# Optimization experiments

Measured on AMD Instinct MI355X. Metric: run time of the kernel, lower is better.

Reference implementation:

```python
import jax, jax.numpy as jnp
import numpy as np

EMBED_DIM = 1024
NUM_HEADS = 16
HEAD_DIM = EMBED_DIM // NUM_HEADS


def setup_inputs() -> dict:
    key = jax.random.key(0)
    k_x, k_wqkv, k_bqkv, k_wo, k_bo = jax.random.split(key, 5)
    b, n = 2, 2048
    scale_in = 1.0 / np.sqrt(EMBED_DIM)
    return {
        "x": jax.random.normal(k_x, (b, n, EMBED_DIM), dtype=jnp.float32),
        "W_qkv": jax.random.normal(k_wqkv, (EMBED_DIM, 3 * EMBED_DIM), dtype=jnp.float32) * scale_in,
        "b_qkv": jnp.zeros((3 * EMBED_DIM,), dtype=jnp.float32),
        "W_out": jax.random.normal(k_wo, (EMBED_DIM, EMBED_DIM), dtype=jnp.float32) * scale_in,
        "b_out": jnp.zeros((EMBED_DIM,), dtype=jnp.float32),
    }


def _rope_rotate(t, cos, sin):
    # t: [b, h, n, hd]; cos/sin: [1, 1, n, hd//2]
    t1, t2 = jnp.split(t, 2, axis=-1)
    return jnp.concatenate([cos * t1 - sin * t2, sin * t1 + cos * t2], axis=-1)


def reference(x, W_qkv, b_qkv, W_out, b_out):
    b, n, d = x.shape
    h, hd = NUM_HEADS, HEAD_DIM

    qkv = x @ W_qkv + b_qkv                      # [b, n, 3d]
    q, k, v = jnp.split(qkv, 3, axis=-1)
    q, k, v = [t.reshape(b, n, h, hd).transpose(0, 2, 1, 3) for t in (q, k, v)]

    # RoPE tables
    hd2 = hd // 2
    theta = 10000.0 ** (-2.0 * jnp.arange(hd2, dtype=jnp.float32) / hd)
    freqs = jnp.arange(n, dtype=jnp.float32)[:, None] * theta[None, :]  # [n, hd2]
    cos = jnp.cos(freqs)[None, None]
    sin = jnp.sin(freqs)[None, None]
    q = _rope_rotate(q, cos, sin)
    k = _rope_rotate(k, cos, sin)

    scores = jnp.einsum('bhqd,bhkd->bhqk', q, k) / jnp.sqrt(jnp.float32(hd))
    attn = jax.nn.softmax(scores, axis=-1)       # [b, h, n, n]
    out = jnp.einsum('bhqk,bhkd->bhqd', attn, v)
    out = out.transpose(0, 2, 1, 3).reshape(b, n, d)
    return out @ W_out + b_out
```

## Files before the change

kernel.cpp:

```cpp
#include <hip/hip_runtime.h>
#include <hip/hip_bf16.h>
#include <math.h>

#define EMBED 1024
#define NHEAD 16
#define HD 64
#define BATCH 2
#define SEQ 2048
#define MTOT (BATCH * SEQ)
#define QKVN (3 * EMBED)

typedef __attribute__((ext_vector_type(8))) short short8;
typedef __attribute__((ext_vector_type(4))) float f32x4;

typedef __attribute__((address_space(1))) const unsigned int GUI;
typedef __attribute__((address_space(3))) unsigned int LUI;

__device__ __forceinline__ void gload_lds16(const void* src, void* dst) {
  __builtin_amdgcn_global_load_lds((GUI*)src, (LUI*)dst, 16, 0, 0);
}

__device__ __forceinline__ unsigned short f2bf(float f) {
  unsigned u = __builtin_bit_cast(unsigned, f);
  u += 0x7fffu + ((u >> 16) & 1u);
  return (unsigned short)(u >> 16);
}

__device__ __forceinline__ unsigned cvt_pk_bf16(float lo, float hi) {
  unsigned r;
  asm("v_cvt_pk_bf16_f32 %0, %1, %2" : "=v"(r) : "v"(lo), "v"(hi));
  return r;
}

#define QSCALE 0.1803368801111191f


__global__ __launch_bounds__(256) void k_cvt(const float* __restrict__ in,
                                             unsigned short* __restrict__ out, int n4) {
  int i = blockIdx.x * 256 + threadIdx.x;
  if (i >= n4) return;
  float4 v = reinterpret_cast<const float4*>(in)[i];
  ushort4 o;
  o.x = f2bf(v.x); o.y = f2bf(v.y); o.z = f2bf(v.z); o.w = f2bf(v.w);
  reinterpret_cast<ushort4*>(out)[i] = o;
}

__global__ __launch_bounds__(256) void k_transpose_cvt(const float* __restrict__ W,
                                                       unsigned short* __restrict__ WT,
                                                       int K, int Ncols) {
  __shared__ float tile[32][33];
  int n0 = blockIdx.x * 32, k0 = blockIdx.y * 32;
  int tc = threadIdx.x & 31, tr = threadIdx.x >> 5;
  for (int i = 0; i < 4; i++) {
    int r = tr + i * 8;
    tile[r][tc] = W[(size_t)(k0 + r) * Ncols + n0 + tc];
  }
  __syncthreads();
  for (int i = 0; i < 4; i++) {
    int r = tr + i * 8;
    WT[(size_t)(n0 + r) * K + k0 + tc] = f2bf(tile[tc][r]);
  }
}

__global__ __launch_bounds__(256) void k_rope_tables(float* __restrict__ cosT,
                                                     float* __restrict__ sinT) {
  int idx = blockIdx.x * 256 + threadIdx.x;
  if (idx >= SEQ * 32) return;
  int pos = idx >> 5, i = idx & 31;
  float theta = __expf((float)i * -0.28782313662425575f);
  float f = (float)pos * theta;
  cosT[idx] = cosf(f);
  sinT[idx] = sinf(f);
}

__device__ __forceinline__ void gemm_mainloop(const unsigned short* __restrict__ A,
                                              const unsigned short* __restrict__ Bt,
                                              unsigned short* Al, unsigned short* Bl,
                                              size_t m0, size_t n0,
                                              int tid, int l15, int g, int wm, int wn,
                                              f32x4 acc[4][4]) {
  const int w = tid >> 6;
  const int lane = tid & 63;
  const int srow = lane >> 3, slot = lane & 7;
  for (int k0 = 0; k0 < 1024; k0 += 64) {
    __syncthreads();
    for (int it = 0; it < 4; it++) {
      const int r = w * 32 + it * 8 + srow;
      const int sc = (slot ^ (r & 7)) * 8;
      gload_lds16(A + (m0 + r) * 1024 + k0 + sc, &Al[(w * 32 + it * 8) * 64]);
      gload_lds16(Bt + (n0 + r) * 1024 + k0 + sc, &Bl[(w * 32 + it * 8) * 64]);
    }
    __syncthreads();
    for (int kk = 0; kk < 2; kk++) {
      short8 fa[4], fb[4];
      const int xr = ((kk * 4 + g) ^ (l15 & 7)) * 8;
      for (int i = 0; i < 4; i++)
        fa[i] = *reinterpret_cast<const short8*>(&Al[(wm * 64 + i * 16 + l15) * 64 + xr]);
      for (int j = 0; j < 4; j++)
        fb[j] = *reinterpret_cast<const short8*>(&Bl[(wn * 64 + j * 16 + l15) * 64 + xr]);
      for (int i = 0; i < 4; i++)
        for (int j = 0; j < 4; j++)
          acc[i][j] = __builtin_amdgcn_mfma_f32_16x16x32_bf16(fa[i], fb[j], acc[i][j], 0, 0, 0);
    }
  }
}

__global__ __launch_bounds__(256) void k_qkv_gemm(const unsigned short* __restrict__ A,
                                                  const unsigned short* __restrict__ Bt,
                                                  const float* __restrict__ bias,
                                                  const float* __restrict__ cosT,
                                                  const float* __restrict__ sinT,
                                                  unsigned short* __restrict__ Qb,
                                                  unsigned short* __restrict__ Kb,
                                                  unsigned short* __restrict__ Vtg) {
  __shared__ alignas(16) unsigned short Al[128 * 64];
  __shared__ alignas(16) unsigned short Bl[128 * 64];
  const int tid = threadIdx.x;
  const int lane = tid & 63, l15 = lane & 15, g = lane >> 4;
  const int wid = tid >> 6, wm = wid >> 1, wn = wid & 1;
  const size_t m0 = (size_t)blockIdx.y * 128;
  const size_t n0 = (size_t)blockIdx.x * 128;
  f32x4 acc[4][4] = {};
  gemm_mainloop(A, Bt, Al, Bl, m0, n0, tid, l15, g, wm, wn, acc);

  const int cbase = (int)n0 + wn * 64;
  const int sec = cbase >> 10;
  const int head = (cbase & 1023) >> 6;
  float bia[4];
  for (int j = 0; j < 4; j++) bia[j] = bias[cbase + j * 16 + l15];
  const size_t mw = m0 + wm * 64;

  if (sec == 2) {
    const int dsw = ((l15 >> 3) & 1) << 2;
    for (int i = 0; i < 4; i++) {
      size_t mbase = mw + i * 16 + g * 4;
      int bb = (int)(mbase >> 11), pos0 = (int)(mbase & 2047);
      size_t hb = (size_t)(bb * NHEAD + head) * HD;
      for (int j = 0; j < 4; j++) {
        int d = j * 16 + l15;
        uint2 pk;
        pk.x = cvt_pk_bf16(acc[i][j][0] + bia[j], acc[i][j][1] + bia[j]);
        pk.y = cvt_pk_bf16(acc[i][j][2] + bia[j], acc[i][j][3] + bia[j]);
        *reinterpret_cast<uint2*>(Vtg + (hb + d) * SEQ + (pos0 ^ dsw)) = pk;
      }
    }
  } else {
    unsigned short* dst = sec ? Kb : Qb;
    const float qs = sec ? 1.0f : QSCALE;
    for (int i = 0; i < 4; i++)
      for (int r = 0; r < 4; r++) {
        size_t m = mw + i * 16 + g * 4 + r;
        int bb = (int)(m >> 11), pos = (int)(m & 2047);
        size_t base = ((size_t)(bb * NHEAD + head) * SEQ + pos) * HD;
        const float* cr = cosT + pos * 32;
        const float* sr = sinT + pos * 32;
        for (int pl = 0; pl < 2; pl++) {
          int ii = pl * 16 + l15;
          float c = cr[ii], s = sr[ii];
          float lo = acc[i][pl][r] + bia[pl];
          float hi = acc[i][pl + 2][r] + bia[pl + 2];
          dst[base + ii]      = f2bf((c * lo - s * hi) * qs);
          dst[base + 32 + ii] = f2bf((s * lo + c * hi) * qs);
        }
      }
  }
}

__global__ __launch_bounds__(256) void k_out_gemm(const unsigned short* __restrict__ A,
                                                  const unsigned short* __restrict__ Bt,
                                                  const float* __restrict__ bias,
                                                  float* __restrict__ out) {
  __shared__ alignas(16) unsigned short Al[128 * 64];
  __shared__ alignas(16) unsigned short Bl[64 * 64];
  const int tid = threadIdx.x;
  const int lane = tid & 63, l15 = lane & 15, g = lane >> 4;
  const int wid = tid >> 6, wm = wid >> 1, wn = wid & 1;
  const int w = wid;
  const int srow = lane >> 3, slot = lane & 7;
  const size_t m0 = (size_t)blockIdx.y * 128;
  const size_t n0 = (size_t)blockIdx.x * 64;
  f32x4 acc[4][2] = {};

  for (int k0 = 0; k0 < 1024; k0 += 64) {
    __syncthreads();
    for (int it = 0; it < 4; it++) {
      const int r = w * 32 + it * 8 + srow;
      const int sc = (slot ^ (r & 7)) * 8;
      gload_lds16(A + (m0 + r) * 1024 + k0 + sc, &Al[(w * 32 + it * 8) * 64]);
    }
    for (int it = 0; it < 2; it++) {
      const int r = w * 16 + it * 8 + srow;
      const int sc = (slot ^ (r & 7)) * 8;
      gload_lds16(Bt + (n0 + r) * 1024 + k0 + sc, &Bl[(w * 16 + it * 8) * 64]);
    }
    __syncthreads();
    for (int kk = 0; kk < 2; kk++) {
      short8 fa[4], fb[2];
      const int xr = ((kk * 4 + g) ^ (l15 & 7)) * 8;
      for (int i = 0; i < 4; i++)
        fa[i] = *reinterpret_cast<const short8*>(&Al[(wm * 64 + i * 16 + l15) * 64 + xr]);
      for (int j = 0; j < 2; j++)
        fb[j] = *reinterpret_cast<const short8*>(&Bl[(wn * 32 + j * 16 + l15) * 64 + xr]);
      for (int i = 0; i < 4; i++)
        for (int j = 0; j < 2; j++)
          acc[i][j] = __builtin_amdgcn_mfma_f32_16x16x32_bf16(fa[i], fb[j], acc[i][j], 0, 0, 0);
    }
  }

  const int cbase = (int)n0 + wn * 32;
  const size_t mw = m0 + wm * 64;
  for (int i = 0; i < 4; i++)
    for (int r = 0; r < 4; r++) {
      size_t m = mw + i * 16 + g * 4 + r;
      for (int j = 0; j < 2; j++) {
        int col = cbase + j * 16 + l15;
        out[m * EMBED + col] = acc[i][j][r] + bias[col];
      }
    }
}

__global__ __launch_bounds__(256) void k_attn(const unsigned short* __restrict__ Q,
                                              const unsigned short* __restrict__ Kg,
                                              const unsigned short* __restrict__ Vtg,
                                              unsigned short* __restrict__ AO) {
  __shared__ alignas(16) unsigned short Kt[64 * 64];
  __shared__ alignas(16) unsigned short Vt[64 * 64];
  const int tid = threadIdx.x, w = tid >> 6, lane = tid & 63;
  const int l15 = lane & 15, g = lane >> 4;
  const int srow = lane >> 3, slot = lane & 7;
  const int bh = blockIdx.y;
  const unsigned short* Qp = Q + (size_t)bh * SEQ * HD;
  const unsigned short* Kp = Kg + (size_t)bh * SEQ * HD;
  const unsigned short* Vp = Vtg + (size_t)bh * HD * SEQ;
  const int q0 = blockIdx.x * 64 + w * 16;

  short8 aq[2];
  for (int kk = 0; kk < 2; kk++)
    aq[kk] = *reinterpret_cast<const short8*>(Qp + (size_t)(q0 + l15) * HD + kk * 32 + g * 8);

  f32x4 o[4] = {};
  float mrow = -INFINITY, lrow = 0.f;

  for (int t = 0; t < SEQ / 64; t++) {
    const int kb = t * 64;
    __syncthreads();
    for (int it = 0; it < 2; it++) {
      const int r = w * 16 + it * 8 + srow;
      const int sc = (slot ^ (r & 7)) * 8;
      gload_lds16(Kp + (size_t)(kb + r) * HD + sc, &Kt[(w * 16 + it * 8) * 64]);
      gload_lds16(Vp + (size_t)r * SEQ + kb + sc, &Vt[(w * 16 + it * 8) * 64]);
    }
    __syncthreads();

    f32x4 s[4] = {};
    __builtin_amdgcn_s_setprio(1);
    for (int kk = 0; kk < 2; kk++) {
      const int xr = ((kk * 4 + g) ^ (l15 & 7)) * 8;
      for (int c = 0; c < 4; c++) {
        short8 ak = *reinterpret_cast<const short8*>(&Kt[(c * 16 + l15) * 64 + xr]);
        s[c] = __builtin_amdgcn_mfma_f32_16x16x32_bf16(ak, aq[kk], s[c], 0, 0, 0);
      }
    }
    __builtin_amdgcn_s_setprio(0);

    float tm = s[0][0];
#pragma unroll
    for (int c = 0; c < 4; c++)
#pragma unroll
      for (int r = 0; r < 4; r++) tm = fmaxf(tm, s[c][r]);
    tm = fmaxf(tm, __shfl_xor(tm, 16, 64));
    tm = fmaxf(tm, __shfl_xor(tm, 32, 64));

    if (!__all(tm <= mrow + 11.5f)) {
      float mn = fmaxf(mrow, tm);
      float fac = __builtin_exp2f(mrow - mn);
      lrow *= fac;
#pragma unroll
      for (int c2 = 0; c2 < 4; c2++)
#pragma unroll
        for (int r = 0; r < 4; r++) o[c2][r] *= fac;
      mrow = mn;
    }

    float rs = 0.f;
    unsigned wpk[8];
#pragma unroll
    for (int c = 0; c < 4; c++) {
      float p0 = __builtin_exp2f(s[c][0] - mrow);
      float p1 = __builtin_exp2f(s[c][1] - mrow);
      float p2 = __builtin_exp2f(s[c][2] - mrow);
      float p3 = __builtin_exp2f(s[c][3] - mrow);
      rs += (p0 + p1) + (p2 + p3);
      wpk[2 * c]     = cvt_pk_bf16(p0, p1);
      wpk[2 * c + 1] = cvt_pk_bf16(p2, p3);
    }
    rs += __shfl_xor(rs, 16, 64);
    rs += __shfl_xor(rs, 32, 64);
    lrow += rs;

    const int rx = l15 & 7;
    const int h4 = ((g ^ (l15 >> 3)) & 1) * 4;
    __builtin_amdgcn_s_setprio(1);
#pragma unroll
    for (int kk = 0; kk < 2; kk++) {
      short8 pb = __builtin_bit_cast(short8,
          uint4{wpk[4 * kk], wpk[4 * kk + 1], wpk[4 * kk + 2], wpk[4 * kk + 3]});
#pragma unroll
      for (int c2 = 0; c2 < 4; c2++) {
        const unsigned short* vrow = &Vt[(c2 * 16 + l15) * 64];
        uint2 v1 = *reinterpret_cast<const uint2*>(vrow + ((4 * kk + (g >> 1)) ^ rx) * 8 + h4);
        uint2 v2 = *reinterpret_cast<const uint2*>(vrow + ((4 * kk + 2 + (g >> 1)) ^ rx) * 8 + h4);
        short8 av = __builtin_bit_cast(short8, uint4{v1.x, v1.y, v2.x, v2.y});
        o[c2] = __builtin_amdgcn_mfma_f32_16x16x32_bf16(av, pb, o[c2], 0, 0, 0);
      }
    }
    __builtin_amdgcn_s_setprio(0);
  }

  const int bb = bh >> 4, h = bh & 15;
  const float inv = 1.f / lrow;
  const int pos = q0 + l15;
  unsigned short* dst = AO + ((size_t)bb * SEQ + pos) * EMBED + h * HD;
#pragma unroll
  for (int c2 = 0; c2 < 4; c2++) {
    uint2 pk;
    pk.x = cvt_pk_bf16(o[c2][0] * inv, o[c2][1] * inv);
    pk.y = cvt_pk_bf16(o[c2][2] * inv, o[c2][3] * inv);
    *reinterpret_cast<uint2*>(dst + c2 * 16 + g * 4) = pk;
  }
}

extern "C" void kernel_launch(void* const* d_in, const int* in_sizes, int n_in,
                              void* d_out, int out_size, void* d_ws, size_t ws_size,
                              hipStream_t stream) {
  const float* x    = (const float*)d_in[0];
  const float* Wqkv = (const float*)d_in[1];
  const float* bqkv = (const float*)d_in[2];
  const float* Wout = (const float*)d_in[3];
  const float* bout = (const float*)d_in[4];
  float* out = (float*)d_out;

  char* ws = (char*)d_ws;
  size_t off = 0;
  auto carve = [&](size_t bytes) {
    char* p = ws + off;
    off += (bytes + 255) & ~(size_t)255;
    return p;
  };
  float* cosT           = (float*)carve((size_t)SEQ * 32 * 4);
  float* sinT           = (float*)carve((size_t)SEQ * 32 * 4);
  unsigned short* Xb    = (unsigned short*)carve((size_t)MTOT * EMBED * 2);
  unsigned short* WqkvT = (unsigned short*)carve((size_t)QKVN * EMBED * 2);
  unsigned short* WoT   = (unsigned short*)carve((size_t)EMBED * EMBED * 2);
  unsigned short* Qb    = (unsigned short*)carve((size_t)MTOT * EMBED * 2);
  unsigned short* Kb    = (unsigned short*)carve((size_t)MTOT * EMBED * 2);
  unsigned short* Vtg   = (unsigned short*)carve((size_t)MTOT * EMBED * 2);
  unsigned short* AO    = (unsigned short*)carve((size_t)MTOT * EMBED * 2);

  k_cvt<<<(MTOT * EMBED / 4 + 255) / 256, 256, 0, stream>>>(x, Xb, MTOT * EMBED / 4);
  k_transpose_cvt<<<dim3(QKVN / 32, EMBED / 32), 256, 0, stream>>>(Wqkv, WqkvT, EMBED, QKVN);
  k_transpose_cvt<<<dim3(EMBED / 32, EMBED / 32), 256, 0, stream>>>(Wout, WoT, EMBED, EMBED);
  k_rope_tables<<<(SEQ * 32) / 256, 256, 0, stream>>>(cosT, sinT);

  k_qkv_gemm<<<dim3(QKVN / 128, MTOT / 128), 256, 0, stream>>>(Xb, WqkvT, bqkv, cosT, sinT, Qb, Kb, Vtg);
  k_attn<<<dim3(SEQ / 64, BATCH * NHEAD), 256, 0, stream>>>(Qb, Kb, Vtg, AO);
  k_out_gemm<<<dim3(EMBED / 64, MTOT / 128), 256, 0, stream>>>(AO, WoT, bout, out);
}
```

Measured before the change: 157.5 us.

## Double-buffer K/V tiles in attention and remap blocks for XCD locality

The attention kernel now prefetches the next K/V tile into a second LDS buffer while computing on the current one, leaving one barrier per iteration instead of two. The grid becomes 1D and block indices are remapped so that all query blocks of a given batch-head land on the same XCD, which should improve L2 reuse of K/V. The setprio hints around the MFMA sections are removed. LDS use doubles, which may reduce occupancy. Correctness depends on the global_load_lds writes being complete when the end-of-iteration barrier is reached.

After: 157.7 us. About the same (+0.1%).

```diff
diff --git a/kernel.cpp b/kernel.cpp
--- a/kernel.cpp
+++ b/kernel.cpp
@@ -223,45 +223,59 @@
                                               const unsigned short* __restrict__ Kg,
                                               const unsigned short* __restrict__ Vtg,
                                               unsigned short* __restrict__ AO) {
-  __shared__ alignas(16) unsigned short Kt[64 * 64];
-  __shared__ alignas(16) unsigned short Vt[64 * 64];
+  __shared__ alignas(16) unsigned short Kt[2][64 * 64];
+  __shared__ alignas(16) unsigned short Vt[2][64 * 64];
   const int tid = threadIdx.x, w = tid >> 6, lane = tid & 63;
   const int l15 = lane & 15, g = lane >> 4;
   const int srow = lane >> 3, slot = lane & 7;
-  const int bh = blockIdx.y;
+
+  const int n = blockIdx.x;
+  const int xcd = n & 7, rest = n >> 3;
+  const int qb = rest & 31, bh = (rest >> 5) * 8 + xcd;
+
   const unsigned short* Qp = Q + (size_t)bh * SEQ * HD;
   const unsigned short* Kp = Kg + (size_t)bh * SEQ * HD;
   const unsigned short* Vp = Vtg + (size_t)bh * HD * SEQ;
-  const int q0 = blockIdx.x * 64 + w * 16;
+  const int q0 = qb * 64 + w * 16;
 
   short8 aq[2];
   for (int kk = 0; kk < 2; kk++)
     aq[kk] = *reinterpret_cast<const short8*>(Qp + (size_t)(q0 + l15) * HD + kk * 32 + g * 8);
 
+  const int sr16 = w * 16 + srow;
+  const int sc0 = (slot ^ (sr16 & 7)) * 8;
+
   f32x4 o[4] = {};
   float mrow = -INFINITY, lrow = 0.f;
+  int cur = 0;
+
+  {
+    gload_lds16(Kp + (size_t)sr16 * HD + sc0, &Kt[0][(w * 16) * 64]);
+    gload_lds16(Vp + (size_t)sr16 * SEQ + sc0, &Vt[0][(w * 16) * 64]);
+    gload_lds16(Kp + (size_t)(sr16 + 8) * HD + sc0, &Kt[0][(w * 16 + 8) * 64]);
+    gload_lds16(Vp + (size_t)(sr16 + 8) * SEQ + sc0, &Vt[0][(w * 16 + 8) * 64]);
+  }
+  __syncthreads();
 
   for (int t = 0; t < SEQ / 64; t++) {
-    const int kb = t * 64;
-    __syncthreads();
-    for (int it = 0; it < 2; it++) {
-      const int r = w * 16 + it * 8 + srow;
-      const int sc = (slot ^ (r & 7)) * 8;
-      gload_lds16(Kp + (size_t)(kb + r) * HD + sc, &Kt[(w * 16 + it * 8) * 64]);
-      gload_lds16(Vp + (size_t)r * SEQ + kb + sc, &Vt[(w * 16 + it * 8) * 64]);
-    }
-    __syncthreads();
+    if (t + 1 < SEQ / 64) {
+      const int kb = (t + 1) * 64;
+      gload_lds16(Kp + (size_t)(kb + sr16) * HD + sc0, &Kt[cur ^ 1][(w * 16) * 64]);
+      gload_lds16(Vp + (size_t)sr16 * SEQ + kb + sc0, &Vt[cur ^ 1][(w * 16) * 64]);
+      gload_lds16(Kp + (size_t)(kb + sr16 + 8) * HD + sc0, &Kt[cur ^ 1][(w * 16 + 8) * 64]);
+      gload_lds16(Vp + (size_t)(sr16 + 8) * SEQ + kb + sc0, &Vt[cur ^ 1][(w * 16 + 8) * 64]);
+    }
+    const unsigned short* Ktc = Kt[cur];
+    const unsigned short* Vtc = Vt[cur];
 
     f32x4 s[4] = {};
-    __builtin_amdgcn_s_setprio(1);
     for (int kk = 0; kk < 2; kk++) {
       const int xr = ((kk * 4 + g) ^ (l15 & 7)) * 8;
       for (int c = 0; c < 4; c++) {
-        short8 ak = *reinterpret_cast<const short8*>(&Kt[(c * 16 + l15) * 64 + xr]);
+        short8 ak = *reinterpret_cast<const short8*>(&Ktc[(c * 16 + l15) * 64 + xr]);
         s[c] = __builtin_amdgcn_mfma_f32_16x16x32_bf16(ak, aq[kk], s[c], 0, 0, 0);
       }
     }
-    __builtin_amdgcn_s_setprio(0);
 
     float tm = s[0][0];
 #pragma unroll
@@ -300,21 +314,22 @@
 
     const int rx = l15 & 7;
     const int h4 = ((g ^ (l15 >> 3)) & 1) * 4;
-    __builtin_amdgcn_s_setprio(1);
 #pragma unroll
     for (int kk = 0; kk < 2; kk++) {
       short8 pb = __builtin_bit_cast(short8,
           uint4{wpk[4 * kk], wpk[4 * kk + 1], wpk[4 * kk + 2], wpk[4 * kk + 3]});
 #pragma unroll
       for (int c2 = 0; c2 < 4; c2++) {
-        const unsigned short* vrow = &Vt[(c2 * 16 + l15) * 64];
+        const unsigned short* vrow = &Vtc[(c2 * 16 + l15) * 64];
         uint2 v1 = *reinterpret_cast<const uint2*>(vrow + ((4 * kk + (g >> 1)) ^ rx) * 8 + h4);
         uint2 v2 = *reinterpret_cast<const uint2*>(vrow + ((4 * kk + 2 + (g >> 1)) ^ rx) * 8 + h4);
         short8 av = __builtin_bit_cast(short8, uint4{v1.x, v1.y, v2.x, v2.y});
         o[c2] = __builtin_amdgcn_mfma_f32_16x16x32_bf16(av, pb, o[c2], 0, 0, 0);
       }
     }
-    __builtin_amdgcn_s_setprio(0);
+
+    __syncthreads();
+    cur ^= 1;
   }
 
   const int bb = bh >> 4, h = bh & 15;
@@ -363,6 +378,6 @@
   k_rope_tables<<<(SEQ * 32) / 256, 256, 0, stream>>>(cosT, sinT);
 
   k_qkv_gemm<<<dim3(QKVN / 128, MTOT / 128), 256, 0, stream>>>(Xb, WqkvT, bqkv, cosT, sinT, Qb, Kb, Vtg);
-  k_attn<<<dim3(SEQ / 64, BATCH * NHEAD), 256, 0, stream>>>(Qb, Kb, Vtg, AO);
+  k_attn<<<dim3(32 * 32), 256, 0, stream>>>(Qb, Kb, Vtg, AO);
   k_out_gemm<<<dim3(EMBED / 64, MTOT / 128), 256, 0, stream>>>(AO, WoT, bout, out);
 }
```
